# Performance work log

Measured on AMD Instinct MI355X. Metric: run time of the kernel, lower is better.

## Reference

```python
import jax, jax.numpy as jnp
import numpy as np

CUTOFF = 5.0
ENV_EXP = 5          # envelope_exponent
NUM_RADIAL = 6
EMB = 128
NUM_ATOM_TYPES = 95
N_NODES = 50000
N_EDGES = 800000


def envelope(x):
    # p = exponent + 1
    p = ENV_EXP + 1
    a = -(p + 1) * (p + 2) / 2.0
    b = p * (p + 2) * 1.0
    c = -p * (p + 1) / 2.0
    x_p_0 = x ** (p - 1)
    x_p_1 = x_p_0 * x
    x_p_2 = x_p_1 * x
    return 1.0 / x + a * x_p_0 + b * x_p_1 + c * x_p_2


def setup_inputs() -> dict:
    key = jax.random.key(0)
    ks = jax.random.split(key, 10)
    Z = jax.random.randint(ks[0], (N_NODES,), 0, NUM_ATOM_TYPES)
    src = jax.random.randint(ks[1], (N_EDGES,), 0, N_NODES)
    dst = jax.random.randint(ks[2], (N_EDGES,), 0, N_NODES)
    rbf = jax.random.normal(ks[3], (N_EDGES, NUM_RADIAL), dtype=jnp.float32)
    # distances in (0, cutoff]; keep away from 0 to avoid 1/x blowup
    d = jax.random.uniform(ks[4], (N_EDGES,), dtype=jnp.float32,
                           minval=0.05, maxval=1.0) * CUTOFF
    sqrt3 = float(np.sqrt(3.0))
    emb_table = jax.random.uniform(ks[5], (NUM_ATOM_TYPES, EMB),
                                   dtype=jnp.float32, minval=-sqrt3, maxval=sqrt3)
    W_rbf = jax.random.normal(ks[6], (EMB, NUM_RADIAL), dtype=jnp.float32) * (1.0 / np.sqrt(NUM_RADIAL))
    b_rbf = jnp.zeros((EMB,), dtype=jnp.float32)
    W_dense = jax.random.normal(ks[7], (EMB, 3 * EMB), dtype=jnp.float32) * (1.0 / np.sqrt(3 * EMB))
    b_dense = jnp.zeros((EMB,), dtype=jnp.float32)
    return {"Z": Z, "src": src, "dst": dst, "rbf": rbf, "d": d,
            "emb_table": emb_table, "W_rbf": W_rbf, "b_rbf": b_rbf,
            "W_dense": W_dense, "b_dense": b_dense}


def reference(Z, src, dst, rbf, d, emb_table, W_rbf, b_rbf, W_dense, b_dense):
    act = jax.nn.silu
    # node embeddings: g.ndata['h'] = embedding(Z)
    h = emb_table[Z]                                   # [N, EMB]
    # edge_init
    rbf_proj = act(rbf @ W_rbf.T + b_rbf)              # [E, EMB]
    m = jnp.concatenate([h[src], h[dst], rbf_proj], axis=-1)  # [E, 3*EMB]
    m = act(m @ W_dense.T + b_dense)                   # [E, EMB]
    d_scaled = d / CUTOFF                              # [E]
    # bessel funcs: sin(n*pi*x)/x, n = 1..NUM_RADIAL (stacked along dim=1)
    freqs = jnp.pi * jnp.arange(1, NUM_RADIAL + 1, dtype=d.dtype)  # [R]
    rbf_env = jnp.sin(d_scaled[:, None] * freqs) / d_scaled[:, None]  # [E, R]
    d_cutoff = envelope(d_scaled)                      # [E]
    rbf_env = d_cutoff[:, None] * rbf_env              # [E, R]
    return h, m, rbf_env
```

## Files before the change

### kernel.cpp

```cpp
#include <hip/hip_runtime.h>
#include <hip/hip_bf16.h>
#include <math.h>

#define CUTOFFV 5.0f
#define NRAD 6
#define EMB 128
#define NTYPES 95
#define PI_F 3.14159265358979323846f

typedef short short8 __attribute__((ext_vector_type(8)));
typedef float f32x4 __attribute__((ext_vector_type(4)));
typedef float f32x2 __attribute__((ext_vector_type(2)));

__device__ __forceinline__ unsigned short f2bf(float f) {
    union { float f; unsigned int u; } v; v.f = f;
    unsigned int u = v.u;
    unsigned int r = (u + 0x7FFFu + ((u >> 16) & 1u)) >> 16;
    return (unsigned short)r;
}

__device__ __forceinline__ float fast_rcp(float x) {
    float y;
    asm("v_rcp_f32 %0, %1" : "=v"(y) : "v"(x));
    return y;
}

__device__ __forceinline__ float silu_f(float x) {
    return x * fast_rcp(1.0f + __expf(-x));
}

__device__ __forceinline__ float rdlane(float v, int l) {
    return __int_as_float(__builtin_amdgcn_readlane(__float_as_int(v), l));
}

__device__ __forceinline__ void lds_barrier() {
    __builtin_amdgcn_sched_barrier(0);
    asm volatile("s_waitcnt lgkmcnt(0)\n\ts_barrier" ::: "memory");
    __builtin_amdgcn_sched_barrier(0);
}

__global__ void prep_kernel(const float* __restrict__ emb,
                            const float* __restrict__ Wd,
                            const float* __restrict__ bd,
                            const float* __restrict__ Wr,
                            const float* __restrict__ brbf,
                            float* __restrict__ P1, float* __restrict__ P2,
                            unsigned short* __restrict__ W3b,
                            float* __restrict__ Wrp) {
    int b = blockIdx.x, tid = threadIdx.x;
    if (b < 2 * NTYPES) {
        int t = b / NTYPES, z = b % NTYPES;
        __shared__ float emb_s[EMB];
        emb_s[tid] = emb[z * EMB + tid];
        __syncthreads();
        float acc = (t == 0) ? bd[tid] : 0.0f;
        const float* wrow = Wd + (size_t)tid * 384 + t * EMB;
        #pragma unroll 8
        for (int j = 0; j < EMB; ++j) acc += emb_s[j] * wrow[j];
        (t == 0 ? P1 : P2)[z * EMB + tid] = acc;
    } else if (b < 2 * NTYPES + 8) {
        int g = (b - 2 * NTYPES) * 128 + tid;
        for (int i = g; i < EMB * EMB; i += 8 * 128) {
            int n = i >> 7, k = i & 127;
            W3b[i] = f2bf(Wd[(size_t)n * 384 + 256 + k]);
        }
    } else {
        if (tid < EMB) {
            int k = tid;
            #pragma unroll
            for (int j = 0; j < 6; ++j) Wrp[k * 8 + j] = Wr[k * 6 + j];
            Wrp[k * 8 + 6] = brbf[k];
            Wrp[k * 8 + 7] = 0.0f;
        }
    }
}

__global__ void h_kernel(const int* __restrict__ Z, const float* __restrict__ emb,
                         float* __restrict__ out_h, int N) {
    int idx = blockIdx.x * 256 + threadIdx.x;
    int total = N * (EMB / 4);
    if (idx >= total) return;
    int v = idx >> 5, c = idx & 31;
    int z = Z[v];
    const f32x4* e4 = (const f32x4*)emb;
    f32x4* o4 = (f32x4*)out_h;
    o4[idx] = e4[z * 32 + c];
}

__global__ void __launch_bounds__(256, 4)
edge_kernel(const int* __restrict__ Z, const int* __restrict__ src,
            const int* __restrict__ dst, const float* __restrict__ rbf,
            const float* __restrict__ dvec,
            const float* __restrict__ P1, const float* __restrict__ P2,
            const unsigned short* __restrict__ W3b,
            const float* __restrict__ Wrp,
            float* __restrict__ out_m, float* __restrict__ out_env,
            int E, int ntiles) {
    __shared__ unsigned char A_lds[2][64 * 256];
    __shared__ int zs_s[2][64], zd_s[2][64];

    const int tid = threadIdx.x;
    const int lane = tid & 63;
    const int w = tid >> 6;
    const int lr = lane & 15;
    const int lg = lane >> 4;

    const f32x4 cw = ((const f32x4*)Wrp)[tid];

    short8 wfrag[2][4];
    #pragma unroll
    for (int nt = 0; nt < 2; ++nt) {
        int n = w * 32 + nt * 16 + lr;
        #pragma unroll
        for (int ks = 0; ks < 4; ++ks)
            wfrag[nt][ks] = *(const short8*)(W3b + n * EMB + ks * 32 + lg * 8);
    }

    for (int i = 0; ; ++i) {
        const int tp = blockIdx.x + i * gridDim.x;
        const int tc = tp - gridDim.x;
        const bool do_p = (tp < ntiles);
        const bool do_c = (i > 0) && (tc < ntiles);
        if (!do_p && !do_c) break;
        const int pi = i & 1, ci = pi ^ 1;

        f32x2 ra = {0.f, 0.f}, rb = {0.f, 0.f}, rc = {0.f, 0.f};
        float dv = 0.0f;
        int srcv = 0, dstv = 0;
        if (do_p) {
            const int e0p = tp * 64;
            int ecl = e0p + lane; if (ecl >= E) ecl = E - 1;
            const f32x2* r2 = (const f32x2*)(rbf + (size_t)ecl * 6);
            ra = r2[0]; rb = r2[1]; rc = r2[2];
            if (tid < 64) {
                int ec = (e0p + tid < E) ? (e0p + tid) : (E - 1);
                srcv = src[ec]; dstv = dst[ec];
                dv = dvec[ec];
            }
        }

        if (do_c) {
            const int e0c = tc * 64;
            const unsigned char* Ab = A_lds[ci];
            #pragma unroll
            for (int et = 0; et < 4; ++et) {
                const int e_row = et * 16 + lr;
                short8 bfrag[4];
                #pragma unroll
                for (int ks = 0; ks < 4; ++ks) {
                    int off = (e_row * 256 + (ks * 32 + lg * 8) * 2) ^ ((e_row & 7) << 4);
                    bfrag[ks] = *(const short8*)(Ab + off);
                }
                f32x4 acc[2];
                acc[0] = (f32x4){0.f, 0.f, 0.f, 0.f};
                acc[1] = (f32x4){0.f, 0.f, 0.f, 0.f};
                #pragma unroll
                for (int ks = 0; ks < 4; ++ks)
                    #pragma unroll
                    for (int nt = 0; nt < 2; ++nt)
                        acc[nt] = __builtin_amdgcn_mfma_f32_16x16x32_bf16(
                            wfrag[nt][ks], bfrag[ks], acc[nt], 0, 0, 0);

                const int el = e_row;
                const int e = e0c + el;
                const int zs = zs_s[ci][el], zd = zd_s[ci][el];
                #pragma unroll
                for (int nt = 0; nt < 2; ++nt) {
                    int n4 = w * 32 + nt * 16 + lg * 4;
                    const f32x4 p1 = *(const f32x4*)(P1 + zs * EMB + n4);
                    const f32x4 p2 = *(const f32x4*)(P2 + zd * EMB + n4);
                    f32x4 o;
                    o.x = silu_f(acc[nt][0] + p1.x + p2.x);
                    o.y = silu_f(acc[nt][1] + p1.y + p2.y);
                    o.z = silu_f(acc[nt][2] + p1.z + p2.z);
                    o.w = silu_f(acc[nt][3] + p1.w + p2.w);
                    if (e < E)
                        __builtin_nontemporal_store(
                            o, (f32x4*)(out_m + (size_t)e * EMB + n4));
                }
            }
        }

        if (do_p) {
            const int e0p = tp * 64;

            int zsr = 0, zdr = 0;
            if (tid < 64) {
                zsr = Z[srcv]; zdr = Z[dstv];
                int e = e0p + tid;
                if (e < E) {
                    float x = dv * (1.0f / CUTOFFV);
                    float inv = fast_rcp(x);
                    float x2 = x * x;
                    float x5 = x2 * x2 * x;
                    float env = inv + x5 * (-28.0f + x * (48.0f - 21.0f * x));
                    float s1, c1;
                    __sincosf(PI_F * x, &s1, &c1);
                    float twoc = 2.0f * c1;
                    float f = env * inv;
                    float s2 = twoc * s1;
                    float s3 = twoc * s2 - s1;
                    float s4 = twoc * s3 - s2;
                    float s5 = twoc * s4 - s3;
                    float s6 = twoc * s5 - s4;
                    float* o = out_env + (size_t)e * 6;
                    __builtin_nontemporal_store((f32x2){f * s1, f * s2}, (f32x2*)o);
                    __builtin_nontemporal_store((f32x2){f * s3, f * s4}, (f32x2*)(o + 2));
                    __builtin_nontemporal_store((f32x2){f * s5, f * s6}, (f32x2*)(o + 4));
                }
            }

            #pragma unroll
            for (int c = 0; c < 4; ++c) {
                short8 pk;
                #pragma unroll
                for (int j = 0; j < 8; ++j) {
                    const int ln = 2 * (c * 8 + j);
                    float w0 = rdlane(cw.x, ln),     w1 = rdlane(cw.y, ln);
                    float w2 = rdlane(cw.z, ln),     w3v = rdlane(cw.w, ln);
                    float w4 = rdlane(cw.x, ln + 1), w5 = rdlane(cw.y, ln + 1);
                    float bs = rdlane(cw.z, ln + 1);
                    float pre = bs + ra.x * w0 + ra.y * w1 + rb.x * w2 +
                                rb.y * w3v + rc.x * w4 + rc.y * w5;
                    pk[j] = (short)f2bf(silu_f(pre));
                }
                int k0 = w * 32 + c * 8;
                int off = (lane * 256 + k0 * 2) ^ ((lane & 7) << 4);
                *(short8*)(A_lds[pi] + off) = pk;
            }

            if (tid < 64) {
                zs_s[pi][tid] = zsr;
                zd_s[pi][tid] = zdr;
            }
        }

        lds_barrier();
    }
}

extern "C" void kernel_launch(void* const* d_in, const int* in_sizes, int n_in,
                              void* d_out, int out_size, void* d_ws, size_t ws_size,
                              hipStream_t stream) {
    const int* Z = (const int*)d_in[0];
    const int* src = (const int*)d_in[1];
    const int* dst = (const int*)d_in[2];
    const float* rbf = (const float*)d_in[3];
    const float* dvec = (const float*)d_in[4];
    const float* emb = (const float*)d_in[5];
    const float* Wr = (const float*)d_in[6];
    const float* brbf = (const float*)d_in[7];
    const float* Wd = (const float*)d_in[8];
    const float* bd = (const float*)d_in[9];

    const int N = in_sizes[0];
    const int E = in_sizes[1];

    float* out_h = (float*)d_out;
    float* out_m = out_h + (size_t)N * EMB;
    float* out_env = out_m + (size_t)E * EMB;

    float* P1 = (float*)d_ws;
    float* P2 = P1 + NTYPES * EMB;
    unsigned short* W3b = (unsigned short*)(P2 + NTYPES * EMB);
    float* Wrp = (float*)(W3b + EMB * EMB);

    prep_kernel<<<2 * NTYPES + 9, 128, 0, stream>>>(emb, Wd, bd, Wr, brbf,
                                                    P1, P2, W3b, Wrp);

    int hblocks = (N * (EMB / 4) + 255) / 256;
    h_kernel<<<hblocks, 256, 0, stream>>>(Z, emb, out_h, N);

    int ntiles = (E + 63) / 64;
    int grid = ntiles < 1024 ? ntiles : 1024;
    edge_kernel<<<grid, 256, 0, stream>>>(Z, src, dst, rbf, dvec,
                                          P1, P2, W3b, Wrp,
                                          out_m, out_env, E, ntiles);
}
```

Before: 174.7 us.

## Split envelope into its own kernel, single-buffer edge kernel with register prefetch

Moves the Bessel/envelope computation out of the edge kernel into a separate env_kernel. The edge kernel changes from a double-buffered LDS produce/consume pipeline to a single LDS buffer with two barriers per tile, prefetching the next tile's rbf and src/dst indices into registers. It also raises occupancy to 7 blocks per CU with a grid of 1792, reads the rbf-projection weights through wave-uniform scalar loads instead of readlane, and uses the library bf16 conversion. This adds a kernel launch and an extra barrier per tile, and loses the overlap between MFMA work and producer work within a block.

```diff
diff --git a/kernel.cpp b/kernel.cpp
--- a/kernel.cpp
+++ b/kernel.cpp
@@ -19,6 +19,12 @@
     return (unsigned short)r;
 }
 
+__device__ __forceinline__ short bf16s(float f) {
+    union { __hip_bfloat16 h; short s; } u;
+    u.h = __float2bfloat16(f);
+    return u.s;
+}
+
 __device__ __forceinline__ float fast_rcp(float x) {
     float y;
     asm("v_rcp_f32 %0, %1" : "=v"(y) : "v"(x));
@@ -27,10 +33,6 @@
 
 __device__ __forceinline__ float silu_f(float x) {
     return x * fast_rcp(1.0f + __expf(-x));
-}
-
-__device__ __forceinline__ float rdlane(float v, int l) {
-    return __int_as_float(__builtin_amdgcn_readlane(__float_as_int(v), l));
 }
 
 __device__ __forceinline__ void lds_barrier() {
@@ -87,25 +89,47 @@
     o4[idx] = e4[z * 32 + c];
 }
 
-__global__ void __launch_bounds__(256, 4)
+__global__ void env_kernel(const float* __restrict__ dvec,
+                           float* __restrict__ out_env, int E) {
+    int e = blockIdx.x * 256 + threadIdx.x;
+    if (e >= E) return;
+    float x = dvec[e] * (1.0f / CUTOFFV);
+    float inv = fast_rcp(x);
+    float x2 = x * x;
+    float x5 = x2 * x2 * x;
+    float env = inv + x5 * (-28.0f + x * (48.0f - 21.0f * x));
+    float s1, c1;
+    __sincosf(PI_F * x, &s1, &c1);
+    float twoc = 2.0f * c1;
+    float f = env * inv;
+    float s2 = twoc * s1;
+    float s3 = twoc * s2 - s1;
+    float s4 = twoc * s3 - s2;
+    float s5 = twoc * s4 - s3;
+    float s6 = twoc * s5 - s4;
+    float* o = out_env + (size_t)e * 6;
+    __builtin_nontemporal_store((f32x2){f * s1, f * s2}, (f32x2*)o);
+    __builtin_nontemporal_store((f32x2){f * s3, f * s4}, (f32x2*)(o + 2));
+    __builtin_nontemporal_store((f32x2){f * s5, f * s6}, (f32x2*)(o + 4));
+}
+
+__global__ void __launch_bounds__(256, 7)
 edge_kernel(const int* __restrict__ Z, const int* __restrict__ src,
             const int* __restrict__ dst, const float* __restrict__ rbf,
-            const float* __restrict__ dvec,
             const float* __restrict__ P1, const float* __restrict__ P2,
             const unsigned short* __restrict__ W3b,
             const float* __restrict__ Wrp,
-            float* __restrict__ out_m, float* __restrict__ out_env,
+            float* __restrict__ out_m,
             int E, int ntiles) {
-    __shared__ unsigned char A_lds[2][64 * 256];
-    __shared__ int zs_s[2][64], zd_s[2][64];
+    __shared__ unsigned char A_lds[64 * 256];
+    __shared__ int zs_s[64], zd_s[64];
 
     const int tid = threadIdx.x;
     const int lane = tid & 63;
     const int w = tid >> 6;
     const int lr = lane & 15;
     const int lg = lane >> 4;
-
-    const f32x4 cw = ((const f32x4*)Wrp)[tid];
+    const int wu = __builtin_amdgcn_readfirstlane(w);
 
     short8 wfrag[2][4];
     #pragma unroll
@@ -116,126 +140,101 @@
             wfrag[nt][ks] = *(const short8*)(W3b + n * EMB + ks * 32 + lg * 8);
     }
 
-    for (int i = 0; ; ++i) {
-        const int tp = blockIdx.x + i * gridDim.x;
-        const int tc = tp - gridDim.x;
-        const bool do_p = (tp < ntiles);
-        const bool do_c = (i > 0) && (tc < ntiles);
-        if (!do_p && !do_c) break;
-        const int pi = i & 1, ci = pi ^ 1;
-
-        f32x2 ra = {0.f, 0.f}, rb = {0.f, 0.f}, rc = {0.f, 0.f};
-        float dv = 0.0f;
-        int srcv = 0, dstv = 0;
-        if (do_p) {
-            const int e0p = tp * 64;
-            int ecl = e0p + lane; if (ecl >= E) ecl = E - 1;
+    f32x2 ra, rb, rc;
+    int iv = 0;
+    {
+        const int e0p = blockIdx.x * 64;
+        int ecl = e0p + lane; if (ecl >= E) ecl = E - 1;
+        const f32x2* r2 = (const f32x2*)(rbf + (size_t)ecl * 6);
+        ra = r2[0]; rb = r2[1]; rc = r2[2];
+        if (tid < 128) {
+            int ec = e0p + (tid & 63); if (ec >= E) ec = E - 1;
+            iv = (tid < 64) ? src[ec] : dst[ec];
+        }
+    }
+
+    for (int t = blockIdx.x; t < ntiles; t += gridDim.x) {
+        const int tn = t + gridDim.x;
+
+        f32x2 nra, nrb, nrc;
+        int niv = 0;
+        if (tn < ntiles) {
+            const int e0n = tn * 64;
+            int ecl = e0n + lane; if (ecl >= E) ecl = E - 1;
             const f32x2* r2 = (const f32x2*)(rbf + (size_t)ecl * 6);
-            ra = r2[0]; rb = r2[1]; rc = r2[2];
-            if (tid < 64) {
-                int ec = (e0p + tid < E) ? (e0p + tid) : (E - 1);
-                srcv = src[ec]; dstv = dst[ec];
-                dv = dvec[ec];
-            }
-        }
-
-        if (do_c) {
-            const int e0c = tc * 64;
-            const unsigned char* Ab = A_lds[ci];
-            #pragma unroll
-            for (int et = 0; et < 4; ++et) {
-                const int e_row = et * 16 + lr;
-                short8 bfrag[4];
+            nra = r2[0]; nrb = r2[1]; nrc = r2[2];
+            if (tid < 128) {
+                int ec = e0n + (tid & 63); if (ec >= E) ec = E - 1;
+                niv = (tid < 64) ? src[ec] : dst[ec];
+            }
+        }
+
+        int zreg = 0;
+        if (tid < 128) zreg = Z[iv];
+
+        #pragma unroll
+        for (int c = 0; c < 4; ++c) {
+            const float* wp0 = Wrp + (size_t)(wu * 32 + c * 8) * 8;
+            short8 pk;
+            #pragma unroll
+            for (int j = 0; j < 8; ++j) {
+                const float* wp = wp0 + j * 8;
+                float pre = wp[6] + ra.x * wp[0] + ra.y * wp[1] +
+                            rb.x * wp[2] + rb.y * wp[3] +
+                            rc.x * wp[4] + rc.y * wp[5];
+                pk[j] = bf16s(silu_f(pre));
+            }
+            int k0 = wu * 32 + c * 8;
+            int off = (lane * 256 + k0 * 2) ^ ((lane & 7) << 4);
+            *(short8*)(A_lds + off) = pk;
+        }
+        if (tid < 64) zs_s[tid] = zreg;
+        else if (tid < 128) zd_s[tid - 64] = zreg;
+
+        lds_barrier();
+
+        const int e0c = t * 64;
+        #pragma unroll
+        for (int et = 0; et < 4; ++et) {
+            const int e_row = et * 16 + lr;
+            short8 bfrag[4];
+            #pragma unroll
+            for (int ks = 0; ks < 4; ++ks) {
+                int off = (e_row * 256 + (ks * 32 + lg * 8) * 2) ^ ((e_row & 7) << 4);
+                bfrag[ks] = *(const short8*)(A_lds + off);
+            }
+            f32x4 acc[2];
+            acc[0] = (f32x4){0.f, 0.f, 0.f, 0.f};
+            acc[1] = (f32x4){0.f, 0.f, 0.f, 0.f};
+            #pragma unroll
+            for (int ks = 0; ks < 4; ++ks)
                 #pragma unroll
-                for (int ks = 0; ks < 4; ++ks) {
-                    int off = (e_row * 256 + (ks * 32 + lg * 8) * 2) ^ ((e_row & 7) << 4);
-                    bfrag[ks] = *(const short8*)(Ab + off);
-                }
-                f32x4 acc[2];
-                acc[0] = (f32x4){0.f, 0.f, 0.f, 0.f};
-                acc[1] = (f32x4){0.f, 0.f, 0.f, 0.f};
-                #pragma unroll
-                for (int ks = 0; ks < 4; ++ks)
-                    #pragma unroll
-                    for (int nt = 0; nt < 2; ++nt)
-                        acc[nt] = __builtin_amdgcn_mfma_f32_16x16x32_bf16(
-                            wfrag[nt][ks], bfrag[ks], acc[nt], 0, 0, 0);
-
-                const int el = e_row;
-                const int e = e0c + el;
-                const int zs = zs_s[ci][el], zd = zd_s[ci][el];
-                #pragma unroll
-                for (int nt = 0; nt < 2; ++nt) {
-                    int n4 = w * 32 + nt * 16 + lg * 4;
-                    const f32x4 p1 = *(const f32x4*)(P1 + zs * EMB + n4);
-                    const f32x4 p2 = *(const f32x4*)(P2 + zd * EMB + n4);
-                    f32x4 o;
-                    o.x = silu_f(acc[nt][0] + p1.x + p2.x);
-                    o.y = silu_f(acc[nt][1] + p1.y + p2.y);
-                    o.z = silu_f(acc[nt][2] + p1.z + p2.z);
-                    o.w = silu_f(acc[nt][3] + p1.w + p2.w);
-                    if (e < E)
-                        __builtin_nontemporal_store(
-                            o, (f32x4*)(out_m + (size_t)e * EMB + n4));
-                }
-            }
-        }
-
-        if (do_p) {
-            const int e0p = tp * 64;
-
-            int zsr = 0, zdr = 0;
-            if (tid < 64) {
-                zsr = Z[srcv]; zdr = Z[dstv];
-                int e = e0p + tid;
-                if (e < E) {
-                    float x = dv * (1.0f / CUTOFFV);
-                    float inv = fast_rcp(x);
-                    float x2 = x * x;
-                    float x5 = x2 * x2 * x;
-                    float env = inv + x5 * (-28.0f + x * (48.0f - 21.0f * x));
-                    float s1, c1;
-                    __sincosf(PI_F * x, &s1, &c1);
-                    float twoc = 2.0f * c1;
-                    float f = env * inv;
-                    float s2 = twoc * s1;
-                    float s3 = twoc * s2 - s1;
-                    float s4 = twoc * s3 - s2;
-                    float s5 = twoc * s4 - s3;
-                    float s6 = twoc * s5 - s4;
-                    float* o = out_env + (size_t)e * 6;
-                    __builtin_nontemporal_store((f32x2){f * s1, f * s2}, (f32x2*)o);
-                    __builtin_nontemporal_store((f32x2){f * s3, f * s4}, (f32x2*)(o + 2));
-                    __builtin_nontemporal_store((f32x2){f * s5, f * s6}, (f32x2*)(o + 4));
-                }
-            }
-
-            #pragma unroll
-            for (int c = 0; c < 4; ++c) {
-                short8 pk;
-                #pragma unroll
-                for (int j = 0; j < 8; ++j) {
-                    const int ln = 2 * (c * 8 + j);
-                    float w0 = rdlane(cw.x, ln),     w1 = rdlane(cw.y, ln);
-                    float w2 = rdlane(cw.z, ln),     w3v = rdlane(cw.w, ln);
-                    float w4 = rdlane(cw.x, ln + 1), w5 = rdlane(cw.y, ln + 1);
-                    float bs = rdlane(cw.z, ln + 1);
-                    float pre = bs + ra.x * w0 + ra.y * w1 + rb.x * w2 +
-                                rb.y * w3v + rc.x * w4 + rc.y * w5;
-                    pk[j] = (short)f2bf(silu_f(pre));
-                }
-                int k0 = w * 32 + c * 8;
-                int off = (lane * 256 + k0 * 2) ^ ((lane & 7) << 4);
-                *(short8*)(A_lds[pi] + off) = pk;
-            }
-
-            if (tid < 64) {
-                zs_s[pi][tid] = zsr;
-                zd_s[pi][tid] = zdr;
+                for (int nt = 0; nt < 2; ++nt)
+                    acc[nt] = __builtin_amdgcn_mfma_f32_16x16x32_bf16(
+                        wfrag[nt][ks], bfrag[ks], acc[nt], 0, 0, 0);
+
+            const int el = e_row;
+            const int e = e0c + el;
+            const int zs = zs_s[el], zd = zd_s[el];
+            #pragma unroll
+            for (int nt = 0; nt < 2; ++nt) {
+                int n4 = w * 32 + nt * 16 + lg * 4;
+                const f32x4 p1 = *(const f32x4*)(P1 + zs * EMB + n4);
+                const f32x4 p2 = *(const f32x4*)(P2 + zd * EMB + n4);
+                f32x4 o;
+                o.x = silu_f(acc[nt][0] + p1.x + p2.x);
+                o.y = silu_f(acc[nt][1] + p1.y + p2.y);
+                o.z = silu_f(acc[nt][2] + p1.z + p2.z);
+                o.w = silu_f(acc[nt][3] + p1.w + p2.w);
+                if (e < E)
+                    __builtin_nontemporal_store(
+                        o, (f32x4*)(out_m + (size_t)e * EMB + n4));
             }
         }
 
         lds_barrier();
+
+        ra = nra; rb = nrb; rc = nrc; iv = niv;
     }
 }
 
@@ -271,9 +270,12 @@
     int hblocks = (N * (EMB / 4) + 255) / 256;
     h_kernel<<<hblocks, 256, 0, stream>>>(Z, emb, out_h, N);
 
+    int eblocks = (E + 255) / 256;
+    env_kernel<<<eblocks, 256, 0, stream>>>(dvec, out_env, E);
+
     int ntiles = (E + 63) / 64;
-    int grid = ntiles < 1024 ? ntiles : 1024;
-    edge_kernel<<<grid, 256, 0, stream>>>(Z, src, dst, rbf, dvec,
+    int grid = ntiles < 1792 ? ntiles : 1792;
+    edge_kernel<<<grid, 256, 0, stream>>>(Z, src, dst, rbf,
                                           P1, P2, W3b, Wrp,
-                                          out_m, out_env, E, ntiles);
-}
+                                          out_m, E, ntiles);
+}
```

Measured after the change: 189.8 us. 8.7% more time.
